# Performance work log

Measured on AMD Instinct MI355X. Metric: run time of the kernel, lower is better.

Reference implementation:

```python
import jax, jax.numpy as jnp
import numpy as np

B, N, D, NS, ITERS = 32, 2048, 512, 8, 3
EPS = 1e-8
SCALE = D ** -0.5
LN_EPS = 1e-5


def _ln(x, g, b):
    m = x.mean(-1, keepdims=True)
    v = ((x - m) ** 2).mean(-1, keepdims=True)
    return (x - m) * jax.lax.rsqrt(v + LN_EPS) * g + b


def setup_inputs() -> dict:
    key = jax.random.key(0)
    ks = iter(jax.random.split(key, 40))
    w = lambda *s: jax.random.normal(next(ks), s, jnp.float32) * 0.02
    inp = {
        'inputs': jax.random.normal(next(ks), (B, N, D), jnp.float32),
        'slot_noise': jax.random.normal(next(ks), (B, NS, D), jnp.float32),
        'slots_mu': jax.random.normal(next(ks), (1, 1, D), jnp.float32),
        'slots_logsigma': w(1, 1, D),
        'k_w': w(D, D), 'k_b': jnp.zeros((D,), jnp.float32),
        'v_w': w(D, D), 'v_b': jnp.zeros((D,), jnp.float32),
        'gru_w_ih': w(3 * D, D), 'gru_w_hh': w(3 * D, D),
        'gru_b_ih': jnp.zeros((3 * D,), jnp.float32),
        'gru_b_hh': jnp.zeros((3 * D,), jnp.float32),
        'ln_in_g': jnp.ones((D,), jnp.float32), 'ln_in_b': jnp.zeros((D,), jnp.float32),
        'ln_slots_g': jnp.ones((D,), jnp.float32), 'ln_slots_b': jnp.zeros((D,), jnp.float32),
        'ln_pre_g': jnp.ones((D,), jnp.float32), 'ln_pre_b': jnp.zeros((D,), jnp.float32),
        'mlp1_w': w(1024, D), 'mlp1_b': jnp.zeros((1024,), jnp.float32),
        'mlp2_w': w(1024, 1024), 'mlp2_b': jnp.zeros((1024,), jnp.float32),
        'mlp3_w': w(512, 1024), 'mlp3_b': jnp.zeros((512,), jnp.float32),
        'mlp4_w': w(256, 512), 'mlp4_b': jnp.zeros((256,), jnp.float32),
    }
    return inp


def reference(inputs, slot_noise, slots_mu, slots_logsigma, k_w, k_b, v_w, v_b,
              gru_w_ih, gru_w_hh, gru_b_ih, gru_b_hh,
              ln_in_g, ln_in_b, ln_slots_g, ln_slots_b, ln_pre_g, ln_pre_b,
              mlp1_w, mlp1_b, mlp2_w, mlp2_b, mlp3_w, mlp3_b, mlp4_w, mlp4_b):
    b, n, d = inputs.shape
    # stochastic slot init: mu + exp(logsigma) * noise  -> [b, ns, d]
    slots = slots_mu + jnp.exp(slots_logsigma) * slot_noise
    x = _ln(inputs, ln_in_g, ln_in_b)
    k = x @ k_w.T + k_b
    v = x @ v_w.T + v_b
    updates = slots
    for _ in range(ITERS):
        slots_prev = slots
        q = _ln(slots, ln_slots_g, ln_slots_b)
        dots = jnp.einsum('bid,bjd->bij', q, k) * SCALE  # [b, ns, n]
        attn = jax.nn.softmax(dots, axis=1) + EPS        # softmax over slot axis
        attn = attn / attn.sum(-1, keepdims=True)        # renorm over tokens
        updates = jnp.einsum('bjd,bij->bid', v, attn)    # [b, ns, d]
        # GRUCell(updates, slots_prev), then residual add of updates
        u = updates.reshape(-1, d)
        h = slots_prev.reshape(-1, d)
        gi = u @ gru_w_ih.T + gru_b_ih
        gh = h @ gru_w_hh.T + gru_b_hh
        i_r, i_z, i_n = jnp.split(gi, 3, axis=-1)
        h_r, h_z, h_n = jnp.split(gh, 3, axis=-1)
        r = jax.nn.sigmoid(i_r + h_r)
        z = jax.nn.sigmoid(i_z + h_z)
        nn_ = jnp.tanh(i_n + r * h_n)
        h_new = (1.0 - z) * nn_ + z * h
        slots = (u + h_new).reshape(b, -1, d)
    # output MLP with exact GELU (torch default)
    s = _ln(slots, ln_pre_g, ln_pre_b)
    s = jax.nn.gelu(s @ mlp1_w.T + mlp1_b, approximate=False)
    s = jax.nn.gelu(s @ mlp2_w.T + mlp2_b, approximate=False)
    s = jax.nn.gelu(s @ mlp3_w.T + mlp3_b, approximate=False)
    s = s @ mlp4_w.T + mlp4_b
    return (updates, s)
```

## Files before the change

### kernel.cpp

```cpp
#include <hip/hip_runtime.h>
#include <math.h>

#define Bb 32
#define Nn 2048
#define Dd 512
#define NS 8
#define ITERS 3
#define EPSf 1e-8f
#define SCALEf 0.04419417382415922f
#define LN_EPSf 1e-5f

#define CHUNKS 16
#define SUBT 32

typedef _Float16 half8 __attribute__((ext_vector_type(8)));
typedef _Float16 half2v __attribute__((ext_vector_type(2)));
typedef float f32x4 __attribute__((ext_vector_type(4)));

__device__ __forceinline__ float waveReduceSum(float v) {
    #pragma unroll
    for (int m = 32; m >= 1; m >>= 1) v += __shfl_xor(v, m);
    return v;
}

__device__ __forceinline__ float gelu_exact(float x) {
    return 0.5f * x * (1.0f + erff(x * 0.7071067811865476f));
}

__device__ __forceinline__ void async_copy16(const _Float16* g, _Float16* l) {
    __builtin_amdgcn_global_load_lds(
        (const __attribute__((address_space(1))) unsigned int*)g,
        (__attribute__((address_space(3))) unsigned int*)l, 16, 0, 0);
}

__global__ __launch_bounds__(256) void megapack_kernel(
    const float* __restrict__ w_ih, const float* __restrict__ w_hh,
    const float* __restrict__ m1, const float* __restrict__ m2,
    const float* __restrict__ m3, const float* __restrict__ m4,
    const float* __restrict__ v_w,
    _Float16* __restrict__ Bih, _Float16* __restrict__ Bhh,
    _Float16* __restrict__ Bm1, _Float16* __restrict__ Bm2,
    _Float16* __restrict__ Bm3, _Float16* __restrict__ Bm4,
    _Float16* __restrict__ Bvd) {
    int bid = blockIdx.x, tid = threadIdx.x;
    const float* src; _Float16* dst; int kbits, base;
    if      (bid < 3072)  { src = w_ih; dst = Bih; kbits = 9;  base = 0; }
    else if (bid < 6144)  { src = w_hh; dst = Bhh; kbits = 9;  base = 3072; }
    else if (bid < 8192)  { src = m1;   dst = Bm1; kbits = 9;  base = 6144; }
    else if (bid < 12288) { src = m2;   dst = Bm2; kbits = 10; base = 8192; }
    else if (bid < 14336) { src = m3;   dst = Bm3; kbits = 10; base = 12288; }
    else if (bid < 14848) { src = m4;   dst = Bm4; kbits = 9;  base = 14336; }
    else                  { src = v_w;  dst = Bvd; kbits = 9;  base = 14848; }
    int e = (bid - base) * 256 + tid;
    int K = 1 << kbits;
    int row = e >> kbits, k = e & (K - 1);
    _Float16 h = (_Float16)src[e];
    _Float16* d = dst + ((size_t)row << (kbits + 1));
    d[k] = h;
    d[K + k] = h;
}

__global__ __launch_bounds__(256) void kwt_kernel(
    const float* __restrict__ kw, _Float16* __restrict__ BkT) {
    __shared__ float t[64][65];
    const int bf = blockIdx.x * 64, bd = blockIdx.y * 64;
    const int tid = threadIdx.x;
    #pragma unroll
    for (int i = 0; i < 16; ++i) {
        int idx = i * 256 + tid;
        int r = idx >> 6, c = idx & 63;
        t[r][c] = kw[(size_t)(bf + r) * 512 + bd + c];
    }
    __syncthreads();
    #pragma unroll
    for (int i = 0; i < 16; ++i) {
        int idx = i * 256 + tid;
        int r = idx >> 6, c = idx & 63;
        BkT[(size_t)(bd + r) * 512 + bf + c] = (_Float16)t[c][r];
    }
}

__global__ __launch_bounds__(256) void pack_ln_single_kernel(
    const float* __restrict__ x, const float* __restrict__ g, const float* __restrict__ b,
    _Float16* __restrict__ Ap) {
    int wid = blockIdx.x * 4 + (threadIdx.x >> 6);
    int lane = threadIdx.x & 63;
    const float4* row4 = (const float4*)(x + (size_t)wid * Dd);
    float4 va = row4[lane * 2], vb = row4[lane * 2 + 1];
    float v[8] = {va.x, va.y, va.z, va.w, vb.x, vb.y, vb.z, vb.w};
    float s = 0.f, sq = 0.f;
    #pragma unroll
    for (int t = 0; t < 8; ++t) { s += v[t]; sq += v[t] * v[t]; }
    s = waveReduceSum(s);
    sq = waveReduceSum(sq);
    float m = s * (1.0f / Dd);
    float var = sq * (1.0f / Dd) - m * m;
    float rs = rsqrtf(var + LN_EPSf);
    const float4* g4 = (const float4*)g;
    const float4* b4 = (const float4*)b;
    float4 ga = g4[lane * 2], gb = g4[lane * 2 + 1];
    float4 ba = b4[lane * 2], bb = b4[lane * 2 + 1];
    float gg[8] = {ga.x, ga.y, ga.z, ga.w, gb.x, gb.y, gb.z, gb.w};
    float bbv[8] = {ba.x, ba.y, ba.z, ba.w, bb.x, bb.y, bb.z, bb.w};
    half8 o;
    #pragma unroll
    for (int t = 0; t < 8; ++t) o[t] = (_Float16)((v[t] - m) * rs * gg[t] + bbv[t]);
    *(half8*)(Ap + (size_t)wid * Dd + lane * 8) = o;
}

__global__ __launch_bounds__(256) void slots_init_kernel(
    const float* __restrict__ noise, const float* __restrict__ mu,
    const float* __restrict__ ls, float* __restrict__ slots, _Float16* __restrict__ A2,
    const float* __restrict__ lns_g, const float* __restrict__ lns_b,
    _Float16* __restrict__ qh, const float* __restrict__ k_b, float* __restrict__ cvec) {
    int row = blockIdx.x * 4 + (threadIdx.x >> 6);
    int lane = threadIdx.x & 63;
    float val[8];
    float s = 0.f, sq = 0.f;
    #pragma unroll
    for (int t = 0; t < 8; ++t) {
        int d = t * 64 + lane;
        float v = mu[d] + expf(ls[d]) * noise[(size_t)row * 512 + d];
        val[t] = v;
        s += v; sq += v * v;
        slots[(size_t)row * 512 + d] = v;
        _Float16 hi = (_Float16)v;
        A2[(size_t)(256 + row) * 1024 + d] = hi;
        A2[(size_t)(256 + row) * 1024 + 512 + d] = (_Float16)(v - (float)hi);
    }
    s = waveReduceSum(s);
    sq = waveReduceSum(sq);
    float m = s * (1.0f / Dd);
    float var = sq * (1.0f / Dd) - m * m;
    float rs = rsqrtf(var + LN_EPSf);
    float c = 0.f;
    #pragma unroll
    for (int t = 0; t < 8; ++t) {
        int d = t * 64 + lane;
        float qv = ((val[t] - m) * rs * lns_g[d] + lns_b[d]) * SCALEf;
        qh[(size_t)row * 512 + d] = (_Float16)qv;
        c += qv * k_b[d];
    }
    c = waveReduceSum(c);
    if (lane == 0) cvec[row] = c;
}

__global__ __launch_bounds__(256) void attn_kernel(
    const _Float16* __restrict__ Apack, const _Float16* __restrict__ Qk,
    const float* __restrict__ cvec,
    float* __restrict__ rawp, float* __restrict__ sumsp) {
    const int b = blockIdx.y, chunk = blockIdx.x;
    __shared__ _Float16 Xs[2][SUBT * 512];
    __shared__ _Float16 aTh[SUBT][8];
    __shared__ float dlo[SUBT][8];
    __shared__ float sred[2][8];
    const int tid = threadIdx.x, w = tid >> 6, lane = tid & 63;
    const int lr = lane & 15, quad = lane >> 4;
    const int mt = w & 1, hl = w >> 1;
    const size_t tokbase = (size_t)b * Nn + chunk * 128;

    const float cv = cvec[b * 8 + (lr & 7)];
    const _Float16* qkrow = Qk + ((size_t)(b * 8 + (lr & 7)) << 10) + hl * 512;

    float2 w8[8];
    #pragma unroll
    for (int s = 0; s < 8; ++s) w8[s] = (float2){0.f, 0.f};
    float ssum_part = 0.f;
    const int d0 = w * 128 + lane * 2;
    const int pvslot = d0 >> 3, pvsub = d0 & 7;

    auto STAGE = [&](int st, int buf) {
        #pragma unroll
        for (int i = 0; i < 8; ++i) {
            int row = i * 4 + w;
            const _Float16* src = Apack + (tokbase + st * SUBT + row) * 512 +
                                  ((lane ^ (row & 7)) << 3);
            async_copy16(src, &Xs[buf][row * 512]);
        }
    };

    STAGE(0, 0);
    for (int st = 0; st < 4; ++st) {
        const int cur = st & 1;
        STAGE(st < 3 ? st + 1 : 3, cur ^ 1);
        asm volatile("s_waitcnt vmcnt(8)" ::: "memory");
        __syncthreads();
        const _Float16* Xc = &Xs[cur][0];
        f32x4 dots = (f32x4){0.f, 0.f, 0.f, 0.f};
        const int rr = mt * 16 + lr;
        #pragma unroll
        for (int ks = 0; ks < 16; ++ks) {
            half8 ax = *(const half8*)(Xc + rr * 512 +
                       ((((ks << 2) | quad) ^ (rr & 7)) << 3));
            half8 bq = *(const half8*)(qkrow + ks * 32 + quad * 8);
            dots = __builtin_amdgcn_mfma_f32_16x16x32_f16(ax, bq, dots, 0, 0, 0);
        }
        if (hl == 1 && lr < 8) {
            #pragma unroll
            for (int r = 0; r < 4; ++r) dlo[mt * 16 + quad * 4 + r][lr] = dots[r];
        }
        __syncthreads();
        if (hl == 0) {
            f32x4 d;
            #pragma unroll
            for (int r = 0; r < 4; ++r)
                d[r] = dots[r] + dlo[mt * 16 + quad * 4 + r][lr & 7] + cv;
            f32x4 mx = d;
            #pragma unroll
            for (int msk = 1; msk <= 4; msk <<= 1) {
                #pragma unroll
                for (int r = 0; r < 4; ++r) mx[r] = fmaxf(mx[r], __shfl_xor(mx[r], msk));
            }
            f32x4 p;
            #pragma unroll
            for (int r = 0; r < 4; ++r) p[r] = __expf(d[r] - mx[r]);
            f32x4 sm = p;
            #pragma unroll
            for (int msk = 1; msk <= 4; msk <<= 1) {
                #pragma unroll
                for (int r = 0; r < 4; ++r) sm[r] += __shfl_xor(sm[r], msk);
            }
            #pragma unroll
            for (int r = 0; r < 4; ++r) {
                _Float16 ph = (_Float16)(p[r] / sm[r] + EPSf);
                if (lr < 8) aTh[mt * 16 + quad * 4 + r][lr] = ph;
                ssum_part += (float)ph;
            }
        }
        __syncthreads();
        #pragma unroll 4
        for (int t = 0; t < SUBT; ++t) {
            half8 aa = *(const half8*)&aTh[t][0];
            half2v xv = *(const half2v*)(Xc + t * 512 +
                        ((pvslot ^ (t & 7)) << 3) + pvsub);
            float x0 = (float)xv[0], x1 = (float)xv[1];
            #pragma unroll
            for (int s = 0; s < 8; ++s) {
                float av = (float)aa[s];
                w8[s].x += av * x0;
                w8[s].y += av * x1;
            }
        }
        __syncthreads();
    }
    asm volatile("s_waitcnt vmcnt(0)" ::: "memory");

    float* rp = rawp + ((size_t)chunk * Bb + b) * NS * Dd + d0;
    #pragma unroll
    for (int s = 0; s < 8; ++s) *(float2*)(rp + s * Dd) = w8[s];

    ssum_part += __shfl_xor(ssum_part, 16);
    ssum_part += __shfl_xor(ssum_part, 32);
    if (hl == 0 && lane < 8) sred[w][lane] = ssum_part;
    __syncthreads();
    if (tid < 8) sumsp[((size_t)chunk * Bb + b) * NS + tid] = sred[0][tid] + sred[1][tid];
}

__global__ __launch_bounds__(256) void finalize_kernel(
    const float* __restrict__ rawp, const float* __restrict__ sumsp,
    _Float16* __restrict__ Whl) {
    int idx = blockIdx.x * 256 + threadIdx.x;
    int row = idx >> 9, d = idx & 511;
    float rs = 0.f, ss = 0.f;
    #pragma unroll
    for (int c = 0; c < CHUNKS; ++c) {
        rs += rawp[(size_t)c * 131072 + idx];
        ss += sumsp[c * 256 + row];
    }
    float val = rs / ss;
    _Float16 hi = (_Float16)val;
    Whl[(size_t)row * 1024 + d] = hi;
    Whl[(size_t)row * 1024 + 512 + d] = (_Float16)(val - (float)hi);
}

__device__ __forceinline__ void hgemm64_core(
    const _Float16* __restrict__ A, const _Float16* __restrict__ Bw,
    int K2, f32x4 acc[2][2], _Float16* As, _Float16* Bs) {
    const int tid = threadIdx.x;
    const int w = tid >> 6, lane = tid & 63;
    const int r8 = lane >> 3, seg = lane & 7;
    const int lr = lane & 15, quad = lane >> 4;
    const int wm = w >> 1, wn = w & 1;
    for (int k0 = 0; k0 < K2; k0 += 64) {
        __syncthreads();
        #pragma unroll
        for (int p = 0; p < 2; ++p) {
            int grp = p * 4 + w;
            int row = grp * 8 + r8;
            async_copy16(A + (size_t)row * K2 + k0 + seg * 8, As + grp * 512);
            async_copy16(Bw + (size_t)row * K2 + k0 + seg * 8, Bs + grp * 512);
        }
        __syncthreads();
        #pragma unroll
        for (int kk = 0; kk < 2; ++kk) {
            half8 a[2], b[2];
            #pragma unroll
            for (int t = 0; t < 2; ++t) {
                a[t] = *(const half8*)(As + (wm * 32 + t * 16 + lr) * 64 + kk * 32 + quad * 8);
                b[t] = *(const half8*)(Bs + (wn * 32 + t * 16 + lr) * 64 + kk * 32 + quad * 8);
            }
            #pragma unroll
            for (int mt = 0; mt < 2; ++mt)
                #pragma unroll
                for (int nt = 0; nt < 2; ++nt)
                    acc[mt][nt] = __builtin_amdgcn_mfma_f32_16x16x32_f16(
                        a[mt], b[nt], acc[mt][nt], 0, 0, 0);
        }
    }
}

template <int ACT, int PACK, int BIAS>
__global__ __launch_bounds__(256) void hgemm64_kernel(
    const _Float16* __restrict__ A, const _Float16* __restrict__ Bw,
    const float* __restrict__ bias, float* __restrict__ C, _Float16* __restrict__ P,
    int K2, int N, int Kp) {
    __shared__ _Float16 As[4096], Bs[4096];
    const int m0 = blockIdx.y * 64, n0 = blockIdx.x * 64;
    f32x4 acc[2][2];
    #pragma unroll
    for (int i = 0; i < 2; ++i)
        #pragma unroll
        for (int j = 0; j < 2; ++j) acc[i][j] = (f32x4){0.f, 0.f, 0.f, 0.f};
    hgemm64_core(A + (size_t)m0 * K2, Bw + (size_t)n0 * K2, K2, acc, As, Bs);
    const int tid = threadIdx.x;
    const int w = tid >> 6, lane = tid & 63;
    const int lr = lane & 15, quad = lane >> 4;
    const int wm = w >> 1, wn = w & 1;
    #pragma unroll
    for (int mt = 0; mt < 2; ++mt)
        #pragma unroll
        for (int nt = 0; nt < 2; ++nt) {
            int n = n0 + wn * 32 + nt * 16 + lr;
            float bv = BIAS ? bias[n] : 0.f;
            #pragma unroll
            for (int r = 0; r < 4; ++r) {
                int m = m0 + wm * 32 + mt * 16 + quad * 4 + r;
                float val = acc[mt][nt][r] + bv;
                if (ACT) val = gelu_exact(val);
                if (PACK) {
                    _Float16 hi = (_Float16)val;
                    P[(size_t)m * 2 * Kp + n] = hi;
                    P[(size_t)m * 2 * Kp + Kp + n] = (_Float16)(val - (float)hi);
                } else {
                    C[(size_t)m * N + n] = val;
                }
            }
        }
}

__global__ __launch_bounds__(256) void ugemm_kernel(
    const _Float16* __restrict__ Whl, const _Float16* __restrict__ Bvd,
    const float* __restrict__ v_b, float* __restrict__ u, float* __restrict__ out0,
    _Float16* __restrict__ A2) {
    __shared__ _Float16 As[4096], Bs[4096];
    const int m0 = blockIdx.y * 64, n0 = blockIdx.x * 64;
    f32x4 acc[2][2];
    #pragma unroll
    for (int i = 0; i < 2; ++i)
        #pragma unroll
        for (int j = 0; j < 2; ++j) acc[i][j] = (f32x4){0.f, 0.f, 0.f, 0.f};
    hgemm64_core(Whl + (size_t)m0 * 1024, Bvd + (size_t)n0 * 1024, 1024, acc, As, Bs);
    const int tid = threadIdx.x;
    const int w = tid >> 6, lane = tid & 63;
    const int lr = lane & 15, quad = lane >> 4;
    const int wm = w >> 1, wn = w & 1;
    #pragma unroll
    for (int mt = 0; mt < 2; ++mt)
        #pragma unroll
        for (int nt = 0; nt < 2; ++nt) {
            int n = n0 + wn * 32 + nt * 16 + lr;
            float bv = v_b[n];
            #pragma unroll
            for (int r = 0; r < 4; ++r) {
                int m = m0 + wm * 32 + mt * 16 + quad * 4 + r;
                float val = acc[mt][nt][r] + bv;
                u[(size_t)m * 512 + n] = val;
                out0[(size_t)m * 512 + n] = val;
                _Float16 hi = (_Float16)val;
                A2[(size_t)m * 1024 + n] = hi;
                A2[(size_t)m * 1024 + 512 + n] = (_Float16)(val - (float)hi);
            }
        }
}

__global__ __launch_bounds__(256) void gru_gemm_kernel(
    const _Float16* __restrict__ A2, const _Float16* __restrict__ Bih,
    const _Float16* __restrict__ Bhh, const float* __restrict__ b_ih,
    const float* __restrict__ b_hh, float* __restrict__ gi, float* __restrict__ gh) {
    __shared__ _Float16 As[4096], Bs[4096];
    const int by = blockIdx.y;
    const int n0 = blockIdx.x * 64;
    const _Float16* Ap; const _Float16* Bw; const float* bias; float* C;
    if (by < 4) { Ap = A2 + (size_t)by * 64 * 1024;        Bw = Bih; bias = b_ih; C = gi + (size_t)by * 64 * 1536; }
    else        { Ap = A2 + (size_t)(256 + (by - 4) * 64) * 1024; Bw = Bhh; bias = b_hh; C = gh + (size_t)(by - 4) * 64 * 1536; }
    f32x4 acc[2][2];
    #pragma unroll
    for (int i = 0; i < 2; ++i)
        #pragma unroll
        for (int j = 0; j < 2; ++j) acc[i][j] = (f32x4){0.f, 0.f, 0.f, 0.f};
    hgemm64_core(Ap, Bw + (size_t)n0 * 1024, 1024, acc, As, Bs);
    const int tid = threadIdx.x;
    const int w = tid >> 6, lane = tid & 63;
    const int lr = lane & 15, quad = lane >> 4;
    const int wm = w >> 1, wn = w & 1;
    #pragma unroll
    for (int mt = 0; mt < 2; ++mt)
        #pragma unroll
        for (int nt = 0; nt < 2; ++nt) {
            int n = n0 + wn * 32 + nt * 16 + lr;
            float bv = bias[n];
            #pragma unroll
            for (int r = 0; r < 4; ++r) {
                int m = wm * 32 + mt * 16 + quad * 4 + r;
                C[(size_t)m * 1536 + n] = acc[mt][nt][r] + bv;
            }
        }
}

__global__ __launch_bounds__(256) void gru_elem_kernel(
    const float* __restrict__ gi, const float* __restrict__ gh,
    const float* __restrict__ u, float* __restrict__ slots, _Float16* __restrict__ A2,
    const float* __restrict__ lns_g, const float* __restrict__ lns_b,
    _Float16* __restrict__ qh, const float* __restrict__ k_b, float* __restrict__ cvec,
    const float* __restrict__ lnp_g, const float* __restrict__ lnp_b,
    _Float16* __restrict__ P1, int last) {
    int row = blockIdx.x * 4 + (threadIdx.x >> 6);
    int lane = threadIdx.x & 63;
    const float* gir = gi + (size_t)row * 1536;
    const float* ghr = gh + (size_t)row * 1536;
    float val[8];
    #pragma unroll
    for (int t = 0; t < 8; ++t) {
        int d = t * 64 + lane;
        float ir = gir[d], iz = gir[512 + d], in_ = gir[1024 + d];
        float hr = ghr[d], hz = ghr[512 + d], hn = ghr[1024 + d];
        float r = 1.0f / (1.0f + expf(-(ir + hr)));
        float z = 1.0f / (1.0f + expf(-(iz + hz)));
        float n = tanhf(in_ + r * hn);
        float h = slots[(size_t)row * 512 + d];
        float hnew = (1.0f - z) * n + z * h;
        float vv = u[(size_t)row * 512 + d] + hnew;
        val[t] = vv;
        slots[(size_t)row * 512 + d] = vv;
        _Float16 hi = (_Float16)vv;
        A2[(size_t)(256 + row) * 1024 + d] = hi;
        A2[(size_t)(256 + row) * 1024 + 512 + d] = (_Float16)(vv - (float)hi);
    }
    float s = 0.f, sq = 0.f;
    #pragma unroll
    for (int t = 0; t < 8; ++t) { s += val[t]; sq += val[t] * val[t]; }
    s = waveReduceSum(s);
    sq = waveReduceSum(sq);
    float m = s * (1.0f / Dd);
    float var = sq * (1.0f / Dd) - m * m;
    float rs = rsqrtf(var + LN_EPSf);
    if (!last) {
        float c = 0.f;
        #pragma unroll
        for (int t = 0; t < 8; ++t) {
            int d = t * 64 + lane;
            float qv = ((val[t] - m) * rs * lns_g[d] + lns_b[d]) * SCALEf;
            qh[(size_t)row * 512 + d] = (_Float16)qv;
            c += qv * k_b[d];
        }
        c = waveReduceSum(c);
        if (lane == 0) cvec[row] = c;
    } else {
        #pragma unroll
        for (int t = 0; t < 8; ++t) {
            int d = t * 64 + lane;
            float a = (val[t] - m) * rs * lnp_g[d] + lnp_b[d];
            _Float16 hi = (_Float16)a;
            P1[(size_t)row * 1024 + d] = hi;
            P1[(size_t)row * 1024 + 512 + d] = (_Float16)(a - (float)hi);
        }
    }
}

extern "C" void kernel_launch(void* const* d_in, const int* in_sizes, int n_in,
                              void* d_out, int out_size, void* d_ws, size_t ws_size,
                              hipStream_t stream) {
    const float* inputs   = (const float*)d_in[0];
    const float* noise    = (const float*)d_in[1];
    const float* mu       = (const float*)d_in[2];
    const float* lsig     = (const float*)d_in[3];
    const float* k_w      = (const float*)d_in[4];
    const float* k_b      = (const float*)d_in[5];
    const float* v_w      = (const float*)d_in[6];
    const float* v_b      = (const float*)d_in[7];
    const float* w_ih     = (const float*)d_in[8];
    const float* w_hh     = (const float*)d_in[9];
    const float* b_ih     = (const float*)d_in[10];
    const float* b_hh     = (const float*)d_in[11];
    const float* ln_in_g  = (const float*)d_in[12];
    const float* ln_in_b  = (const float*)d_in[13];
    const float* ln_s_g   = (const float*)d_in[14];
    const float* ln_s_b   = (const float*)d_in[15];
    const float* ln_p_g   = (const float*)d_in[16];
    const float* ln_p_b   = (const float*)d_in[17];
    const float* mlp1_w   = (const float*)d_in[18];
    const float* mlp1_b   = (const float*)d_in[19];
    const float* mlp2_w   = (const float*)d_in[20];
    const float* mlp2_b   = (const float*)d_in[21];
    const float* mlp3_w   = (const float*)d_in[22];
    const float* mlp3_b   = (const float*)d_in[23];
    const float* mlp4_w   = (const float*)d_in[24];
    const float* mlp4_b   = (const float*)d_in[25];
    float* out0 = (float*)d_out;
    float* out1 = (float*)d_out + Bb * NS * Dd;

    char* wp = (char*)d_ws;
    auto alloc = [&](size_t bytes) -> void* {
        void* p = (void*)wp;
        wp += (bytes + 255) & ~(size_t)255;
        return p;
    };
    const size_t MR = (size_t)Bb * Nn;
    _Float16* Apack = (_Float16*)alloc(MR * 512 * 2);
    _Float16* Bih   = (_Float16*)alloc((size_t)1536 * 1024 * 2);
    _Float16* Bhh   = (_Float16*)alloc((size_t)1536 * 1024 * 2);
    _Float16* Bm1   = (_Float16*)alloc((size_t)1024 * 1024 * 2);
    _Float16* Bm2   = (_Float16*)alloc((size_t)1024 * 2048 * 2);
    _Float16* Bm3   = (_Float16*)alloc((size_t)512 * 2048 * 2);
    _Float16* Bm4   = (_Float16*)alloc((size_t)256 * 1024 * 2);
    _Float16* Bvd   = (_Float16*)alloc((size_t)512 * 1024 * 2);
    _Float16* BkT   = (_Float16*)alloc((size_t)512 * 512 * 2);
    float* slots    = (float*)alloc((size_t)Bb * NS * Dd * 4);
    _Float16* qh    = (_Float16*)alloc((size_t)Bb * NS * Dd * 2);
    float* cvec     = (float*)alloc((size_t)Bb * NS * 4);
    _Float16* Qk    = (_Float16*)alloc((size_t)256 * 1024 * 2);
    float* rawp     = (float*)alloc((size_t)CHUNKS * Bb * NS * Dd * 4);
    float* sumsp    = (float*)alloc((size_t)CHUNKS * Bb * NS * 4);
    _Float16* Whl   = (_Float16*)alloc((size_t)256 * 1024 * 2);
    float* ubuf     = (float*)alloc((size_t)Bb * NS * Dd * 4);
    float* gi       = (float*)alloc((size_t)Bb * NS * 1536 * 4);
    float* gh       = (float*)alloc((size_t)Bb * NS * 1536 * 4);
    _Float16* A2    = (_Float16*)alloc((size_t)512 * 1024 * 2);
    _Float16* P1    = (_Float16*)alloc((size_t)256 * 1024 * 2);
    _Float16* P2    = (_Float16*)alloc((size_t)256 * 2048 * 2);
    _Float16* P3    = (_Float16*)alloc((size_t)256 * 2048 * 2);
    _Float16* P4    = (_Float16*)alloc((size_t)256 * 1024 * 2);

    megapack_kernel<<<15872, 256, 0, stream>>>(
        w_ih, w_hh, mlp1_w, mlp2_w, mlp3_w, mlp4_w, v_w,
        Bih, Bhh, Bm1, Bm2, Bm3, Bm4, Bvd);
    kwt_kernel<<<dim3(8, 8), 256, 0, stream>>>(k_w, BkT);
    pack_ln_single_kernel<<<MR / 4, 256, 0, stream>>>(inputs, ln_in_g, ln_in_b, Apack);
    slots_init_kernel<<<64, 256, 0, stream>>>(noise, mu, lsig, slots, A2,
                                              ln_s_g, ln_s_b, qh, k_b, cvec);

    for (int it = 0; it < ITERS; ++it) {
        hgemm64_kernel<0, 1, 0><<<dim3(8, 4), 256, 0, stream>>>(
            qh, BkT, nullptr, nullptr, Qk, 512, 512, 512);
        attn_kernel<<<dim3(CHUNKS, Bb), 256, 0, stream>>>(Apack, Qk, cvec, rawp, sumsp);
        finalize_kernel<<<512, 256, 0, stream>>>(rawp, sumsp, Whl);
        ugemm_kernel<<<dim3(8, 4), 256, 0, stream>>>(Whl, Bvd, v_b, ubuf, out0, A2);
        gru_gemm_kernel<<<dim3(24, 8), 256, 0, stream>>>(A2, Bih, Bhh, b_ih, b_hh, gi, gh);
        gru_elem_kernel<<<64, 256, 0, stream>>>(gi, gh, ubuf, slots, A2,
                                                ln_s_g, ln_s_b, qh, k_b, cvec,
                                                ln_p_g, ln_p_b, P1, it == ITERS - 1 ? 1 : 0);
    }

    hgemm64_kernel<1, 1, 1><<<dim3(16, 4), 256, 0, stream>>>(P1, Bm1, mlp1_b, nullptr, P2, 1024, 1024, 1024);
    hgemm64_kernel<1, 1, 1><<<dim3(16, 4), 256, 0, stream>>>(P2, Bm2, mlp2_b, nullptr, P3, 2048, 1024, 1024);
    hgemm64_kernel<1, 1, 1><<<dim3(8, 4), 256, 0, stream>>>(P3, Bm3, mlp3_b, nullptr, P4, 2048, 512, 512);
    hgemm64_kernel<0, 0, 1><<<dim3(4, 4), 256, 0, stream>>>(P4, Bm4, mlp4_b, out1, nullptr, 1024, 256, 256);
}
```

Before: 566.5 us.

## Fold v projection into GRU input weights and fuse per-iteration kernels

Precomputes W_ih·W_v once, plus a folded bias, so gi comes straight from the attention weights. The u, gi and gh GEMMs can then run in one launch instead of two dependent ones. Finalize is merged into attn_kernel: a per-batch atomic counter lets the last chunk block do the reduction. This removes two launches and one serial dependency per iteration, at the cost of a one-time folded-weight GEMM and added rounding error from the fp16 pre-multiplied weights.

```diff
diff --git a/kernel.cpp b/kernel.cpp
--- a/kernel.cpp
+++ b/kernel.cpp
@@ -38,13 +38,13 @@
     const float* __restrict__ m1, const float* __restrict__ m2,
     const float* __restrict__ m3, const float* __restrict__ m4,
     const float* __restrict__ v_w,
-    _Float16* __restrict__ Bih, _Float16* __restrict__ Bhh,
+    _Float16* __restrict__ Aih, _Float16* __restrict__ Bhh,
     _Float16* __restrict__ Bm1, _Float16* __restrict__ Bm2,
     _Float16* __restrict__ Bm3, _Float16* __restrict__ Bm4,
     _Float16* __restrict__ Bvd) {
     int bid = blockIdx.x, tid = threadIdx.x;
-    const float* src; _Float16* dst; int kbits, base;
-    if      (bid < 3072)  { src = w_ih; dst = Bih; kbits = 9;  base = 0; }
+    const float* src; _Float16* dst; int kbits, base, hilo = 0;
+    if      (bid < 3072)  { src = w_ih; dst = Aih; kbits = 9;  base = 0; hilo = 1; }
     else if (bid < 6144)  { src = w_hh; dst = Bhh; kbits = 9;  base = 3072; }
     else if (bid < 8192)  { src = m1;   dst = Bm1; kbits = 9;  base = 6144; }
     else if (bid < 12288) { src = m2;   dst = Bm2; kbits = 10; base = 8192; }
@@ -54,30 +54,55 @@
     int e = (bid - base) * 256 + tid;
     int K = 1 << kbits;
     int row = e >> kbits, k = e & (K - 1);
-    _Float16 h = (_Float16)src[e];
+    float v = src[e];
+    _Float16 hi = (_Float16)v;
     _Float16* d = dst + ((size_t)row << (kbits + 1));
-    d[k] = h;
-    d[K + k] = h;
-}
-
-__global__ __launch_bounds__(256) void kwt_kernel(
-    const float* __restrict__ kw, _Float16* __restrict__ BkT) {
+    d[k] = hi;
+    d[K + k] = hilo ? (_Float16)(v - (float)hi) : hi;
+}
+
+__global__ __launch_bounds__(256) void twk_kernel(
+    const float* __restrict__ kw, const float* __restrict__ vw,
+    _Float16* __restrict__ BkT, _Float16* __restrict__ BvT) {
     __shared__ float t[64][65];
+    const int z = blockIdx.z;
+    const float* src = z ? vw : kw;
     const int bf = blockIdx.x * 64, bd = blockIdx.y * 64;
     const int tid = threadIdx.x;
     #pragma unroll
     for (int i = 0; i < 16; ++i) {
         int idx = i * 256 + tid;
         int r = idx >> 6, c = idx & 63;
-        t[r][c] = kw[(size_t)(bf + r) * 512 + bd + c];
+        t[r][c] = src[(size_t)(bf + r) * 512 + bd + c];
     }
     __syncthreads();
     #pragma unroll
     for (int i = 0; i < 16; ++i) {
         int idx = i * 256 + tid;
         int r = idx >> 6, c = idx & 63;
-        BkT[(size_t)(bd + r) * 512 + bf + c] = (_Float16)t[c][r];
-    }
+        _Float16 h = (_Float16)t[c][r];
+        if (z == 0) {
+            BkT[(size_t)(bd + r) * 512 + bf + c] = h;
+        } else {
+            BvT[(size_t)(bd + r) * 1024 + bf + c] = h;
+            BvT[(size_t)(bd + r) * 1024 + 512 + bf + c] = h;
+        }
+    }
+}
+
+__global__ __launch_bounds__(256) void bfih_kernel(
+    const float* __restrict__ w_ih, const float* __restrict__ v_b,
+    const float* __restrict__ b_ih, float* __restrict__ bfih) {
+    int row = blockIdx.x * 4 + (threadIdx.x >> 6);
+    int lane = threadIdx.x & 63;
+    float c = 0.f;
+    #pragma unroll
+    for (int t = 0; t < 8; ++t) {
+        int d = t * 64 + lane;
+        c += w_ih[(size_t)row * 512 + d] * v_b[d];
+    }
+    c = waveReduceSum(c);
+    if (lane == 0) bfih[row] = b_ih[row] + c;
 }
 
 __global__ __launch_bounds__(256) void pack_ln_single_kernel(
@@ -112,7 +137,9 @@
     const float* __restrict__ noise, const float* __restrict__ mu,
     const float* __restrict__ ls, float* __restrict__ slots, _Float16* __restrict__ A2,
     const float* __restrict__ lns_g, const float* __restrict__ lns_b,
-    _Float16* __restrict__ qh, const float* __restrict__ k_b, float* __restrict__ cvec) {
+    _Float16* __restrict__ qh, const float* __restrict__ k_b, float* __restrict__ cvec,
+    unsigned* __restrict__ cnt) {
+    if (blockIdx.x == 0 && threadIdx.x < ITERS * Bb) cnt[threadIdx.x] = 0u;
     int row = blockIdx.x * 4 + (threadIdx.x >> 6);
     int lane = threadIdx.x & 63;
     float val[8];
@@ -148,12 +175,15 @@
 __global__ __launch_bounds__(256) void attn_kernel(
     const _Float16* __restrict__ Apack, const _Float16* __restrict__ Qk,
     const float* __restrict__ cvec,
-    float* __restrict__ rawp, float* __restrict__ sumsp) {
+    float* __restrict__ rawp, float* __restrict__ sumsp,
+    _Float16* __restrict__ Whl, unsigned* __restrict__ cnt, int itc) {
     const int b = blockIdx.y, chunk = blockIdx.x;
     __shared__ _Float16 Xs[2][SUBT * 512];
     __shared__ _Float16 aTh[SUBT][8];
     __shared__ float dlo[SUBT][8];
     __shared__ float sred[2][8];
+    __shared__ int amlast;
+    __shared__ float ssl[8];
     const int tid = threadIdx.x, w = tid >> 6, lane = tid & 63;
     const int lr = lane & 15, quad = lane >> 4;
     const int mt = w & 1, hl = w >> 1;
@@ -254,23 +284,33 @@
     if (hl == 0 && lane < 8) sred[w][lane] = ssum_part;
     __syncthreads();
     if (tid < 8) sumsp[((size_t)chunk * Bb + b) * NS + tid] = sred[0][tid] + sred[1][tid];
-}
-
-__global__ __launch_bounds__(256) void finalize_kernel(
-    const float* __restrict__ rawp, const float* __restrict__ sumsp,
-    _Float16* __restrict__ Whl) {
-    int idx = blockIdx.x * 256 + threadIdx.x;
-    int row = idx >> 9, d = idx & 511;
-    float rs = 0.f, ss = 0.f;
-    #pragma unroll
-    for (int c = 0; c < CHUNKS; ++c) {
-        rs += rawp[(size_t)c * 131072 + idx];
-        ss += sumsp[c * 256 + row];
-    }
-    float val = rs / ss;
-    _Float16 hi = (_Float16)val;
-    Whl[(size_t)row * 1024 + d] = hi;
-    Whl[(size_t)row * 1024 + 512 + d] = (_Float16)(val - (float)hi);
+
+    __threadfence();
+    __syncthreads();
+    if (tid == 0) amlast = (atomicAdd(&cnt[itc * Bb + b], 1u) == CHUNKS - 1);
+    __syncthreads();
+    if (!amlast) return;
+    __threadfence();
+    if (tid < 8) {
+        float ss = 0.f;
+        #pragma unroll
+        for (int c = 0; c < CHUNKS; ++c) ss += sumsp[((size_t)c * Bb + b) * NS + tid];
+        ssl[tid] = ss;
+    }
+    __syncthreads();
+    #pragma unroll
+    for (int t = 0; t < 16; ++t) {
+        int idx = t * 256 + tid;
+        int slot = idx >> 9, d = idx & 511;
+        float acc = 0.f;
+        #pragma unroll
+        for (int c = 0; c < CHUNKS; ++c)
+            acc += rawp[(((size_t)c * Bb + b) * NS + slot) * Dd + d];
+        float val = acc / ssl[slot];
+        _Float16 hi = (_Float16)val;
+        Whl[(size_t)(b * 8 + slot) * 1024 + d] = hi;
+        Whl[(size_t)(b * 8 + slot) * 1024 + 512 + d] = (_Float16)(val - (float)hi);
+    }
 }
 
 __device__ __forceinline__ void hgemm64_core(
@@ -340,7 +380,8 @@
                 if (PACK) {
                     _Float16 hi = (_Float16)val;
                     P[(size_t)m * 2 * Kp + n] = hi;
-                    P[(size_t)m * 2 * Kp + Kp + n] = (_Float16)(val - (float)hi);
+                    P[(size_t)m * 2 * Kp + Kp + n] =
+                        (PACK == 2) ? hi : (_Float16)(val - (float)hi);
                 } else {
                     C[(size_t)m * N + n] = val;
                 }
@@ -348,18 +389,33 @@
         }
 }
 
-__global__ __launch_bounds__(256) void ugemm_kernel(
+__global__ __launch_bounds__(256) void mega_kernel(
     const _Float16* __restrict__ Whl, const _Float16* __restrict__ Bvd,
     const float* __restrict__ v_b, float* __restrict__ u, float* __restrict__ out0,
-    _Float16* __restrict__ A2) {
+    const _Float16* __restrict__ BMih, const float* __restrict__ bfih,
+    float* __restrict__ gi, const _Float16* __restrict__ A2,
+    const _Float16* __restrict__ Bhh, const float* __restrict__ b_hh,
+    float* __restrict__ gh) {
     __shared__ _Float16 As[4096], Bs[4096];
-    const int m0 = blockIdx.y * 64, n0 = blockIdx.x * 64;
+    const int bid = blockIdx.x;
+    const _Float16* Ap; const _Float16* Bw; const float* bias;
+    int m0, n0, role;
+    if (bid < 32) {
+        role = 0; m0 = (bid >> 3) * 64; n0 = (bid & 7) * 64;
+        Ap = Whl + (size_t)m0 * 1024; Bw = Bvd + (size_t)n0 * 1024; bias = v_b;
+    } else if (bid < 128) {
+        role = 1; int idx = bid - 32; m0 = (idx / 24) * 64; n0 = (idx % 24) * 64;
+        Ap = Whl + (size_t)m0 * 1024; Bw = BMih + (size_t)n0 * 1024; bias = bfih;
+    } else {
+        role = 2; int idx = bid - 128; m0 = (idx / 24) * 64; n0 = (idx % 24) * 64;
+        Ap = A2 + (size_t)(256 + m0) * 1024; Bw = Bhh + (size_t)n0 * 1024; bias = b_hh;
+    }
     f32x4 acc[2][2];
     #pragma unroll
     for (int i = 0; i < 2; ++i)
         #pragma unroll
         for (int j = 0; j < 2; ++j) acc[i][j] = (f32x4){0.f, 0.f, 0.f, 0.f};
-    hgemm64_core(Whl + (size_t)m0 * 1024, Bvd + (size_t)n0 * 1024, 1024, acc, As, Bs);
+    hgemm64_core(Ap, Bw, 1024, acc, As, Bs);
     const int tid = threadIdx.x;
     const int w = tid >> 6, lane = tid & 63;
     const int lr = lane & 15, quad = lane >> 4;
@@ -369,50 +425,19 @@
         #pragma unroll
         for (int nt = 0; nt < 2; ++nt) {
             int n = n0 + wn * 32 + nt * 16 + lr;
-            float bv = v_b[n];
+            float bv = bias[n];
             #pragma unroll
             for (int r = 0; r < 4; ++r) {
                 int m = m0 + wm * 32 + mt * 16 + quad * 4 + r;
                 float val = acc[mt][nt][r] + bv;
-                u[(size_t)m * 512 + n] = val;
-                out0[(size_t)m * 512 + n] = val;
-                _Float16 hi = (_Float16)val;
-                A2[(size_t)m * 1024 + n] = hi;
-                A2[(size_t)m * 1024 + 512 + n] = (_Float16)(val - (float)hi);
-            }
-        }
-}
-
-__global__ __launch_bounds__(256) void gru_gemm_kernel(
-    const _Float16* __restrict__ A2, const _Float16* __restrict__ Bih,
-    const _Float16* __restrict__ Bhh, const float* __restrict__ b_ih,
-    const float* __restrict__ b_hh, float* __restrict__ gi, float* __restrict__ gh) {
-    __shared__ _Float16 As[4096], Bs[4096];
-    const int by = blockIdx.y;
-    const int n0 = blockIdx.x * 64;
-    const _Float16* Ap; const _Float16* Bw; const float* bias; float* C;
-    if (by < 4) { Ap = A2 + (size_t)by * 64 * 1024;        Bw = Bih; bias = b_ih; C = gi + (size_t)by * 64 * 1536; }
-    else        { Ap = A2 + (size_t)(256 + (by - 4) * 64) * 1024; Bw = Bhh; bias = b_hh; C = gh + (size_t)(by - 4) * 64 * 1536; }
-    f32x4 acc[2][2];
-    #pragma unroll
-    for (int i = 0; i < 2; ++i)
-        #pragma unroll
-        for (int j = 0; j < 2; ++j) acc[i][j] = (f32x4){0.f, 0.f, 0.f, 0.f};
-    hgemm64_core(Ap, Bw + (size_t)n0 * 1024, 1024, acc, As, Bs);
-    const int tid = threadIdx.x;
-    const int w = tid >> 6, lane = tid & 63;
-    const int lr = lane & 15, quad = lane >> 4;
-    const int wm = w >> 1, wn = w & 1;
-    #pragma unroll
-    for (int mt = 0; mt < 2; ++mt)
-        #pragma unroll
-        for (int nt = 0; nt < 2; ++nt) {
-            int n = n0 + wn * 32 + nt * 16 + lr;
-            float bv = bias[n];
-            #pragma unroll
-            for (int r = 0; r < 4; ++r) {
-                int m = wm * 32 + mt * 16 + quad * 4 + r;
-                C[(size_t)m * 1536 + n] = acc[mt][nt][r] + bv;
+                if (role == 0) {
+                    u[(size_t)m * 512 + n] = val;
+                    out0[(size_t)m * 512 + n] = val;
+                } else if (role == 1) {
+                    gi[(size_t)m * 1536 + n] = val;
+                } else {
+                    gh[(size_t)m * 1536 + n] = val;
+                }
             }
         }
 }
@@ -517,7 +542,7 @@
     };
     const size_t MR = (size_t)Bb * Nn;
     _Float16* Apack = (_Float16*)alloc(MR * 512 * 2);
-    _Float16* Bih   = (_Float16*)alloc((size_t)1536 * 1024 * 2);
+    _Float16* Aih   = (_Float16*)alloc((size_t)1536 * 1024 * 2);
     _Float16* Bhh   = (_Float16*)alloc((size_t)1536 * 1024 * 2);
     _Float16* Bm1   = (_Float16*)alloc((size_t)1024 * 1024 * 2);
     _Float16* Bm2   = (_Float16*)alloc((size_t)1024 * 2048 * 2);
@@ -525,6 +550,10 @@
     _Float16* Bm4   = (_Float16*)alloc((size_t)256 * 1024 * 2);
     _Float16* Bvd   = (_Float16*)alloc((size_t)512 * 1024 * 2);
     _Float16* BkT   = (_Float16*)alloc((size_t)512 * 512 * 2);
+    _Float16* BvT   = (_Float16*)alloc((size_t)512 * 1024 * 2);
+    _Float16* BMih  = (_Float16*)alloc((size_t)1536 * 1024 * 2);
+    float* bfih     = (float*)alloc((size_t)1536 * 4);
+    unsigned* cnt   = (unsigned*)alloc((size_t)ITERS * Bb * 4);
     float* slots    = (float*)alloc((size_t)Bb * NS * Dd * 4);
     _Float16* qh    = (_Float16*)alloc((size_t)Bb * NS * Dd * 2);
     float* cvec     = (float*)alloc((size_t)Bb * NS * 4);
@@ -543,19 +572,22 @@
 
     megapack_kernel<<<15872, 256, 0, stream>>>(
         w_ih, w_hh, mlp1_w, mlp2_w, mlp3_w, mlp4_w, v_w,
-        Bih, Bhh, Bm1, Bm2, Bm3, Bm4, Bvd);
-    kwt_kernel<<<dim3(8, 8), 256, 0, stream>>>(k_w, BkT);
+        Aih, Bhh, Bm1, Bm2, Bm3, Bm4, Bvd);
+    twk_kernel<<<dim3(8, 8, 2), 256, 0, stream>>>(k_w, v_w, BkT, BvT);
     pack_ln_single_kernel<<<MR / 4, 256, 0, stream>>>(inputs, ln_in_g, ln_in_b, Apack);
     slots_init_kernel<<<64, 256, 0, stream>>>(noise, mu, lsig, slots, A2,
-                                              ln_s_g, ln_s_b, qh, k_b, cvec);
+                                              ln_s_g, ln_s_b, qh, k_b, cvec, cnt);
+    bfih_kernel<<<384, 256, 0, stream>>>(w_ih, v_b, b_ih, bfih);
+    hgemm64_kernel<0, 2, 0><<<dim3(8, 24), 256, 0, stream>>>(
+        Aih, BvT, nullptr, nullptr, BMih, 1024, 512, 512);
 
     for (int it = 0; it < ITERS; ++it) {
         hgemm64_kernel<0, 1, 0><<<dim3(8, 4), 256, 0, stream>>>(
             qh, BkT, nullptr, nullptr, Qk, 512, 512, 512);
-        attn_kernel<<<dim3(CHUNKS, Bb), 256, 0, stream>>>(Apack, Qk, cvec, rawp, sumsp);
-        finalize_kernel<<<512, 256, 0, stream>>>(rawp, sumsp, Whl);
-        ugemm_kernel<<<dim3(8, 4), 256, 0, stream>>>(Whl, Bvd, v_b, ubuf, out0, A2);
-        gru_gemm_kernel<<<dim3(24, 8), 256, 0, stream>>>(A2, Bih, Bhh, b_ih, b_hh, gi, gh);
+        attn_kernel<<<dim3(CHUNKS, Bb), 256, 0, stream>>>(
+            Apack, Qk, cvec, rawp, sumsp, Whl, cnt, it);
+        mega_kernel<<<224, 256, 0, stream>>>(
+            Whl, Bvd, v_b, ubuf, out0, BMih, bfih, gi, A2, Bhh, b_hh, gh);
         gru_elem_kernel<<<64, 256, 0, stream>>>(gi, gh, ubuf, slots, A2,
                                                 ln_s_g, ln_s_b, qh, k_b, cvec,
                                                 ln_p_g, ln_p_b, P1, it == ITERS - 1 ? 1 : 0);
```

After: 714.8 us. 26.2% more time.
